# Performance work log

Measured on AMD Instinct MI355X. Metric: run time of the kernel, lower is better.

The kernel has to match this reference:

```python
import jax, jax.numpy as jnp
import numpy as np

EMBED, HEADS, LEVELS, POINTS, MLP = 256, 8, 3, 4, 4
SHAPES = [(60, 80), (30, 40), (15, 20)]  # (H, W) per level


def layer_norm(x, g, b):
    m = jnp.mean(x, -1, keepdims=True)
    v = jnp.mean((x - m) ** 2, -1, keepdims=True)
    return (x - m) * jax.lax.rsqrt(v + 1e-5) * g + b


def _bilinear(v, H, W, gx, gy):
    # v: [B,h,H*W,dh]; gx,gy: [B,h,Nq,P] absolute pixel coords (grid_sample align_corners=False, zero padding)
    x0 = jnp.floor(gx); y0 = jnp.floor(gy)
    wx = gx - x0; wy = gy - y0

    def g(xi, yi):
        valid = ((xi >= 0) & (xi < W) & (yi >= 0) & (yi < H)).astype(v.dtype)
        idx = jnp.clip(yi, 0, H - 1) * W + jnp.clip(xi, 0, W - 1)
        B, h, Nq, P = idx.shape
        out = jnp.take_along_axis(v, idx.reshape(B, h, Nq * P)[..., None], axis=2)
        return out.reshape(B, h, Nq, P, -1) * valid[..., None]

    x0i = x0.astype(jnp.int32); y0i = y0.astype(jnp.int32)
    return (g(x0i, y0i) * ((1 - wx) * (1 - wy))[..., None]
            + g(x0i + 1, y0i) * (wx * (1 - wy))[..., None]
            + g(x0i, y0i + 1) * ((1 - wx) * wy)[..., None]
            + g(x0i + 1, y0i + 1) * (wx * wy)[..., None])


def setup_inputs() -> dict:
    key = jax.random.key(0)
    ks = jax.random.split(key, 16)
    B, Nq, C = 2, 8192, EMBED
    Nv = sum(h * w for h, w in SHAPES)
    s = 0.02
    d = {
        'query': jax.random.normal(ks[0], (B, Nq, C), jnp.float32),
        'value': jax.random.normal(ks[1], (B, Nv, C), jnp.float32),
        'query_pos': jax.random.normal(ks[2], (B, Nq, C), jnp.float32),
        'ref_pts': jax.random.uniform(ks[3], (B, Nq, LEVELS, 2), jnp.float32),
        'spatial_shapes': jnp.array(SHAPES, jnp.int32),
        'level_start_index': jnp.array(np.cumsum([0] + [h * w for h, w in SHAPES[:-1]]), jnp.int32),
        'g1': jnp.ones((C,), jnp.float32), 'b1': jnp.zeros((C,), jnp.float32),
        'Wo': s * jax.random.normal(ks[4], (C, HEADS * LEVELS * POINTS * 2), jnp.float32),
        'bo': jnp.zeros((HEADS * LEVELS * POINTS * 2,), jnp.float32),
        'Wa': s * jax.random.normal(ks[5], (C, HEADS * LEVELS * POINTS), jnp.float32),
        'ba': jnp.zeros((HEADS * LEVELS * POINTS,), jnp.float32),
        'Wv': s * jax.random.normal(ks[6], (C, C), jnp.float32), 'bv': jnp.zeros((C,), jnp.float32),
        'Wp': s * jax.random.normal(ks[7], (C, C), jnp.float32), 'bp': jnp.zeros((C,), jnp.float32),
        'g2': jnp.ones((C,), jnp.float32), 'b2': jnp.zeros((C,), jnp.float32),
        'Wf1': s * jax.random.normal(ks[8], (C, MLP * C), jnp.float32), 'bf1': jnp.zeros((MLP * C,), jnp.float32),
        'Wf2': s * jax.random.normal(ks[9], (MLP * C, C), jnp.float32), 'bf2': jnp.zeros((C,), jnp.float32),
    }
    return d


def reference(query, value, query_pos, ref_pts, spatial_shapes, level_start_index,
              g1, b1, Wo, bo, Wa, ba, Wv, bv, Wp, bp, g2, b2, Wf1, bf1, Wf2, bf2):
    B, Nq, C = query.shape
    dh = C // HEADS
    shapes = np.asarray(spatial_shapes).tolist()
    starts = np.asarray(level_start_index).tolist()

    qn = layer_norm(query, g1, b1)           # pre-norm
    qa = qn + query_pos                       # positional embedding inside attn
    offs = (qa @ Wo + bo).reshape(B, Nq, HEADS, LEVELS, POINTS, 2)
    aw = jax.nn.softmax((qa @ Wa + ba).reshape(B, Nq, HEADS, LEVELS * POINTS), -1)
    aw = aw.reshape(B, Nq, HEADS, LEVELS, POINTS)
    v = (value @ Wv + bv).reshape(B, -1, HEADS, dh).transpose(0, 2, 1, 3)  # [B,h,Nv,dh]

    # offset_normalizer = (W, H) per level
    norm = jnp.array([[w, h] for h, w in shapes], jnp.float32)
    loc = ref_pts[:, :, None, :, None, :] + offs / norm[None, None, None, :, None, :]

    out = jnp.zeros((B, Nq, HEADS, dh), query.dtype)
    for l, (H, W) in enumerate(shapes):
        vl = jax.lax.dynamic_slice_in_dim(v, starts[l], H * W, axis=2)
        gl = loc[:, :, :, l].transpose(0, 2, 1, 3, 4)   # [B,h,Nq,P,2]
        gx = gl[..., 0] * W - 0.5
        gy = gl[..., 1] * H - 0.5
        sampled = _bilinear(vl, H, W, gx, gy)            # [B,h,Nq,P,dh]
        out = out + jnp.einsum('bhqpd,bqhp->bqhd', sampled, aw[:, :, :, l])

    attn = out.reshape(B, Nq, C) @ Wp + bp + qn          # output proj + mmcv internal residual (identity=norm1(query))
    q = query + attn                                     # layer residual
    q2 = layer_norm(q, g2, b2)
    return q + (jax.nn.gelu(q2 @ Wf1 + bf1, approximate=False) @ Wf2 + bf2)
```

## Files before the change

### kernel.cpp

```cpp
#include <hip/hip_runtime.h>
#include <math.h>


typedef short short8 __attribute__((ext_vector_type(8)));
typedef short s16x4 __attribute__((ext_vector_type(4)));
typedef __bf16 bf16x8 __attribute__((ext_vector_type(8)));
typedef float f32x4 __attribute__((ext_vector_type(4)));

__device__ __forceinline__ short f2b(float f) {
  unsigned u = __builtin_bit_cast(unsigned, f);
  u += 0x7fffu + ((u >> 16) & 1u);
  return (short)(u >> 16);
}
__device__ __forceinline__ float b2f(short s) {
  unsigned u = ((unsigned)(unsigned short)s) << 16;
  return __builtin_bit_cast(float, u);
}
__device__ __forceinline__ void b8f(short8 s, float* f) {
  const uint4 u = __builtin_bit_cast(uint4, s);
  f[0] = __builtin_bit_cast(float, u.x << 16);
  f[1] = __builtin_bit_cast(float, u.x & 0xffff0000u);
  f[2] = __builtin_bit_cast(float, u.y << 16);
  f[3] = __builtin_bit_cast(float, u.y & 0xffff0000u);
  f[4] = __builtin_bit_cast(float, u.z << 16);
  f[5] = __builtin_bit_cast(float, u.z & 0xffff0000u);
  f[6] = __builtin_bit_cast(float, u.w << 16);
  f[7] = __builtin_bit_cast(float, u.w & 0xffff0000u);
}

__device__ __forceinline__ f32x4 mfma16(short8 a, short8 b, f32x4 c) {
  return __builtin_amdgcn_mfma_f32_16x16x32_bf16(
      __builtin_bit_cast(bf16x8, a), __builtin_bit_cast(bf16x8, b), c, 0, 0, 0);
}

typedef __attribute__((address_space(3))) unsigned int lds_u32;
typedef const __attribute__((address_space(1))) unsigned int glb_u32;
__device__ __forceinline__ void glds16(const void* g, void* l) {
  __builtin_amdgcn_global_load_lds((glb_u32*)g, (lds_u32*)l, 16, 0, 0);
}

__device__ __forceinline__ float gelu1(float v) {
  return 0.5f * v * (1.f + erff(v * 0.70710678118654752f));
}

template <int EPI>
__device__ __forceinline__ void gemm_core(
    int bx, int by,
    const short* __restrict__ A, const short* __restrict__ Bt,
    const float* __restrict__ bias, const float* __restrict__ bias2,
    const void* __restrict__ add1, const float* __restrict__ add2,
    void* __restrict__ Cout, int M, int Nreal, int ldc, int K, char* smem)
{
  short* sA = (short*)smem;
  short* sB = sA + 8192;
  float* sf = (float*)smem;

  const int t = threadIdx.x;
  const int wave = t >> 6, lane = t & 63;
  const int quad = lane >> 4, l16 = lane & 15;
  const int wm = (wave & 1) * 64, wn = (wave >> 1) * 64;
  const int m0 = by * 128, n0 = bx * 128;

  f32x4 acc[4][4];
#pragma unroll
  for (int i = 0; i < 4; i++)
#pragma unroll
    for (int j = 0; j < 4; j++) acc[i][j] = (f32x4){0.f, 0.f, 0.f, 0.f};

  const int srow = lane >> 3, pos = lane & 7;
  const int chunk = (pos + srow) & 7;
  const short* gA = A + (size_t)(m0 + wave * 32 + srow) * K + chunk * 8;
  const short* gB = Bt + (size_t)(n0 + wave * 32 + srow) * K + chunk * 8;

  const int nk = K >> 6;
  for (int kt = 0; kt < nk; ++kt) {
    if (kt) __syncthreads();
    const int ko = kt * 64;
#pragma unroll
    for (int g = 0; g < 4; ++g) {
      glds16(gA + ko + (size_t)(g * 8) * K, sA + (wave * 32 + g * 8) * 64);
      glds16(gB + ko + (size_t)(g * 8) * K, sB + (wave * 32 + g * 8) * 64);
    }
    __syncthreads();
#pragma unroll
    for (int kk = 0; kk < 2; ++kk) {
      short8 af[4], bf[4];
      const int c = kk * 4 + quad;
#pragma unroll
      for (int i = 0; i < 4; i++) {
        const int lrA = wm + i * 16 + l16;
        af[i] = *(const short8*)&sA[lrA * 64 + ((c - lrA) & 7) * 8];
        const int lrB = wn + i * 16 + l16;
        bf[i] = *(const short8*)&sB[lrB * 64 + ((c - lrB) & 7) * 8];
      }
#pragma unroll
      for (int i = 0; i < 4; i++)
#pragma unroll
        for (int j = 0; j < 4; j++) acc[i][j] = mfma16(bf[j], af[i], acc[i][j]);
    }
  }
  __syncthreads();

#pragma unroll
  for (int b = 0; b < 4; ++b) {
    const bool mine = (b < 2) ? (wm == 0) : (wm == 64);
    if (mine) {
#pragma unroll
      for (int ii = 0; ii < 2; ++ii) {
        const int i = (b & 1) * 2 + ii;
        const int rr = ii * 16 + l16;
#pragma unroll
        for (int j = 0; j < 4; ++j)
          *(f32x4*)&sf[rr * 132 + wn + quad * 4 + j * 16] = acc[i][j];
      }
    }
    __syncthreads();
#pragma unroll
    for (int r2 = 0; r2 < 4; ++r2) {
      const int fidx = r2 * 1024 + t * 4;
      const int row = fidx >> 7, col = fidx & 127;
      const int gm = m0 + b * 32 + row;
      const int cc = n0 + col;
      if (gm < M && cc < Nreal) {
        const float4 v = *(const float4*)&sf[row * 132 + col];
        float4 bb;
        if (EPI == 4) bb = (cc < 192) ? *(const float4*)(bias + cc)
                                      : *(const float4*)(bias2 + cc - 192);
        else bb = *(const float4*)(bias + cc);
        float v0 = v.x + bb.x, v1 = v.y + bb.y, v2 = v.z + bb.z, v3 = v.w + bb.w;
        if (EPI == 1) {
          v0 = gelu1(v0); v1 = gelu1(v1); v2 = gelu1(v2); v3 = gelu1(v3);
          s16x4 o; o.x = f2b(v0); o.y = f2b(v1); o.z = f2b(v2); o.w = f2b(v3);
          *(s16x4*)((short*)Cout + (size_t)gm * ldc + cc) = o;
        } else if (EPI == 5) {
          s16x4 o; o.x = f2b(v0); o.y = f2b(v1); o.z = f2b(v2); o.w = f2b(v3);
          *(s16x4*)((short*)Cout + (size_t)gm * ldc + cc) = o;
        } else {
          if (EPI == 2) {
            const s16x4 a1 = *(const s16x4*)((const short*)add1 + (size_t)gm * ldc + cc);
            v0 += b2f(a1.x); v1 += b2f(a1.y); v2 += b2f(a1.z); v3 += b2f(a1.w);
            const float4 a2 = *(const float4*)(add2 + (size_t)gm * ldc + cc);
            v0 += a2.x; v1 += a2.y; v2 += a2.z; v3 += a2.w;
          } else if (EPI == 3) {
            const float4 a1 = *(const float4*)((const float*)add1 + (size_t)gm * ldc + cc);
            v0 += a1.x; v1 += a1.y; v2 += a1.z; v3 += a1.w;
          }
          *(float4*)((float*)Cout + (size_t)gm * ldc + cc) =
              make_float4(v0, v1, v2, v3);
        }
      }
    }
    __syncthreads();
  }
}

template <int EPI>
__global__ __launch_bounds__(256) void gemm_k(
    const short* __restrict__ A, const short* __restrict__ Bt,
    const float* __restrict__ bias, const float* __restrict__ bias2,
    const void* __restrict__ add1, const float* __restrict__ add2,
    void* __restrict__ Cout, int M, int Nreal, int ldc, int K)
{
  __shared__ __align__(16) char smem[32768];
  gemm_core<EPI>(blockIdx.x, blockIdx.y, A, Bt, bias, bias2, add1, add2,
                 Cout, M, Nreal, ldc, K, smem);
}

__global__ __launch_bounds__(256) void gemm_oa_v(
    const short* __restrict__ qa, const short* __restrict__ wt_oa,
    const float* __restrict__ bo, const float* __restrict__ ba,
    float* __restrict__ oabuf,
    const short* __restrict__ valbf, const short* __restrict__ wt_v,
    const float* __restrict__ bv, short* __restrict__ vproj)
{
  __shared__ __align__(16) char smem[32768];
  const int idx = blockIdx.x;
  if (idx < 384) {
    gemm_core<4>(idx % 3, idx / 3, qa, wt_oa, bo, ba, nullptr, nullptr,
                 oabuf, 16384, 288, 288, 256, smem);
  } else {
    const int r = idx - 384;
    gemm_core<5>(r % 2, r / 2, valbf, wt_v, bv, nullptr, nullptr, nullptr,
                 vproj, 12600, 256, 256, 256, smem);
  }
}

__global__ __launch_bounds__(256) void prep_all(
    const float* __restrict__ Wo, const float* __restrict__ Wa,
    const float* __restrict__ Wv, const float* __restrict__ Wp,
    const float* __restrict__ Wf1, const float* __restrict__ Wf2,
    short* __restrict__ t_oa, short* __restrict__ t_v, short* __restrict__ t_p,
    short* __restrict__ t_f1, short* __restrict__ t_f2,
    const float* __restrict__ value, short* __restrict__ valbf,
    const float* __restrict__ query, const float* __restrict__ query_pos,
    const float* __restrict__ g1, const float* __restrict__ b1,
    short* __restrict__ qnb, short* __restrict__ qa)
{
  __shared__ float tile[32][33];
  const int t = threadIdx.x;
  const int blk = blockIdx.x;

  if (blk < 1792) {
    const int bxa = blk & 255, bya = blk >> 8;
    int K, N, noff; const float* src; short* dst;
    switch (bya) {
      case 0: src = Wo;      dst = t_oa; K = 256;  N = 192;  noff = 0;   break;
      case 1: src = Wa;      dst = t_oa; K = 256;  N = 96;   noff = 192; break;
      case 2: src = nullptr; dst = t_oa; K = 256;  N = 96;   noff = 288; break;
      case 3: src = Wv;      dst = t_v;  K = 256;  N = 256;  noff = 0;   break;
      case 4: src = Wp;      dst = t_p;  K = 256;  N = 256;  noff = 0;   break;
      case 5: src = Wf1;     dst = t_f1; K = 256;  N = 1024; noff = 0;   break;
      default: src = Wf2;    dst = t_f2; K = 1024; N = 256;  noff = 0;   break;
    }
    const int tilesK = K >> 5;
    const int nt = tilesK * (N >> 5);
    if (bxa >= nt) return;
    const int tk = bxa % tilesK, tn = bxa / tilesK;
    const int k0 = tk * 32, n0 = tn * 32;
    const int r = t >> 3, c4 = (t & 7) * 4;
    float4 v = make_float4(0.f, 0.f, 0.f, 0.f);
    if (src) v = *(const float4*)(src + (size_t)(k0 + r) * N + n0 + c4);
    tile[r][c4] = v.x; tile[r][c4 + 1] = v.y; tile[r][c4 + 2] = v.z; tile[r][c4 + 3] = v.w;
    __syncthreads();
    const int nn = t >> 3, kc = (t & 7) * 4;
    s16x4 o;
    o.x = f2b(tile[kc][nn]); o.y = f2b(tile[kc + 1][nn]);
    o.z = f2b(tile[kc + 2][nn]); o.w = f2b(tile[kc + 3][nn]);
    *(s16x4*)(dst + (size_t)(noff + n0 + nn) * K + k0 + kc) = o;
  } else if (blk < 1792 + 3169) {
    const int i = ((blk - 1792) * 256 + t) * 4;
    if (i >= 12672 * 256) return;
    s16x4 o = (s16x4){0, 0, 0, 0};
    if (i < 12600 * 256) {
      float4 v = *(const float4*)(value + i);
      o.x = f2b(v.x); o.y = f2b(v.y); o.z = f2b(v.z); o.w = f2b(v.w);
    }
    *(s16x4*)(valbf + i) = o;
  } else {
    const int row  = (blk - 4961) * 4 + (t >> 6);
    const int lane = t & 63;
    const float4 v = ((const float4*)(query + (size_t)row * 256))[lane];
    float s = v.x + v.y + v.z + v.w;
#pragma unroll
    for (int o = 32; o; o >>= 1) s += __shfl_xor(s, o);
    const float mean = s * (1.f / 256.f);
    const float dx = v.x - mean, dy = v.y - mean, dz = v.z - mean, dw = v.w - mean;
    float s2 = dx * dx + dy * dy + dz * dz + dw * dw;
#pragma unroll
    for (int o = 32; o; o >>= 1) s2 += __shfl_xor(s2, o);
    const float inv = rsqrtf(s2 * (1.f / 256.f) + 1e-5f);
    const float4 gv = ((const float4*)g1)[lane];
    const float4 bv = ((const float4*)b1)[lane];
    const float4 o1 = make_float4(dx * inv * gv.x + bv.x, dy * inv * gv.y + bv.y,
                                  dz * inv * gv.z + bv.z, dw * inv * gv.w + bv.w);
    s16x4 ob; ob.x = f2b(o1.x); ob.y = f2b(o1.y); ob.z = f2b(o1.z); ob.w = f2b(o1.w);
    ((s16x4*)(qnb + (size_t)row * 256))[lane] = ob;
    const float4 pv = ((const float4*)(query_pos + (size_t)row * 256))[lane];
    s16x4 op;
    op.x = f2b(o1.x + pv.x); op.y = f2b(o1.y + pv.y);
    op.z = f2b(o1.z + pv.z); op.w = f2b(o1.w + pv.w);
    ((s16x4*)(qa + (size_t)row * 256))[lane] = op;
  }
}

__global__ __launch_bounds__(256) void ln_kernel(
    const float* __restrict__ x, const float* __restrict__ g,
    const float* __restrict__ bta, short* __restrict__ yb)
{
  const int row  = blockIdx.x * 4 + (threadIdx.x >> 6);
  const int lane = threadIdx.x & 63;
  const float4 v = ((const float4*)(x + (size_t)row * 256))[lane];
  float s = v.x + v.y + v.z + v.w;
#pragma unroll
  for (int o = 32; o; o >>= 1) s += __shfl_xor(s, o);
  const float mean = s * (1.f / 256.f);
  const float dx = v.x - mean, dy = v.y - mean, dz = v.z - mean, dw = v.w - mean;
  float s2 = dx * dx + dy * dy + dz * dz + dw * dw;
#pragma unroll
  for (int o = 32; o; o >>= 1) s2 += __shfl_xor(s2, o);
  const float inv = rsqrtf(s2 * (1.f / 256.f) + 1e-5f);
  const float4 gv = ((const float4*)g)[lane];
  const float4 bv = ((const float4*)bta)[lane];
  s16x4 ob;
  ob.x = f2b(dx * inv * gv.x + bv.x); ob.y = f2b(dy * inv * gv.y + bv.y);
  ob.z = f2b(dz * inv * gv.z + bv.z); ob.w = f2b(dw * inv * gv.w + bv.w);
  ((s16x4*)(yb + (size_t)row * 256))[lane] = ob;
}

__global__ __launch_bounds__(256) void deform_fused(
    const short* __restrict__ vproj, const float* __restrict__ oa,
    const float* __restrict__ refp, short* __restrict__ out)
{
  __shared__ int4 sIdx[768];
  __shared__ s16x4 sW[768];
  const int t = threadIdx.x;

  if (t < 64) {
    const int row = blockIdx.x * 8 + (t >> 3), h = t & 7;
    const float* oarow = oa + (size_t)row * 288;
    float off[24];
    const float4* op = (const float4*)(oarow + h * 24);
#pragma unroll
    for (int i = 0; i < 6; i++) {
      const float4 v = op[i];
      off[i * 4] = v.x; off[i * 4 + 1] = v.y; off[i * 4 + 2] = v.z; off[i * 4 + 3] = v.w;
    }
    float lg[12];
    const float4* ap = (const float4*)(oarow + 192 + h * 12);
#pragma unroll
    for (int i = 0; i < 3; i++) {
      const float4 v = ap[i];
      lg[i * 4] = v.x; lg[i * 4 + 1] = v.y; lg[i * 4 + 2] = v.z; lg[i * 4 + 3] = v.w;
    }
    const float* rp = refp + (size_t)row * 6;
    const float Rx[3] = {rp[0], rp[2], rp[4]}, Ry[3] = {rp[1], rp[3], rp[5]};
    float mx = lg[0];
#pragma unroll
    for (int i = 1; i < 12; i++) mx = fmaxf(mx, lg[i]);
    float sum = 0.f;
#pragma unroll
    for (int i = 0; i < 12; i++) { lg[i] = __expf(lg[i] - mx); sum += lg[i]; }
    const float inv = 1.f / sum;
    const int b = row >> 13;
    const int Hs[3] = {60, 30, 15}, Ws[3] = {80, 40, 20}, St[3] = {0, 4800, 6000};
#pragma unroll
    for (int p = 0; p < 12; p++) {
      const int l = p >> 2;
      const int W = Ws[l], H = Hs[l];
      const float gx = Rx[l] * W + off[p * 2]     - 0.5f;
      const float gy = Ry[l] * H + off[p * 2 + 1] - 0.5f;
      const float x0f = floorf(gx), y0f = floorf(gy);
      const float wx = gx - x0f, wy = gy - y0f;
      const int x0 = (int)x0f, y0 = (int)y0f;
      const float aw = lg[p] * inv;
      float cw[4] = {(1.f - wx) * (1.f - wy), wx * (1.f - wy),
                     (1.f - wx) * wy, wx * wy};
      const int base = b * 6300 + St[l];
      int ci[4];
#pragma unroll
      for (int k = 0; k < 4; k++) {
        const int xx = x0 + (k & 1), yy = y0 + (k >> 1);
        const bool valid = (xx >= 0) & (xx < W) & (yy >= 0) & (yy < H);
        const int xc = min(max(xx, 0), W - 1);
        const int yc = min(max(yy, 0), H - 1);
        ci[k] = ((base + yc * W + xc) << 8) + h * 32;
        cw[k] = valid ? cw[k] * aw : 0.f;
      }
      sIdx[t * 12 + p] = make_int4(ci[0], ci[1], ci[2], ci[3]);
      s16x4 wv; wv.x = f2b(cw[0]); wv.y = f2b(cw[1]); wv.z = f2b(cw[2]); wv.w = f2b(cw[3]);
      sW[t * 12 + p] = wv;
    }
  }
  __syncthreads();

  const int lu = t >> 2, c4 = (t & 3) * 8;
  float acc[8];
#pragma unroll
  for (int i = 0; i < 8; i++) acc[i] = 0.f;
#pragma unroll 2
  for (int p = 0; p < 12; p++) {
    const int4 idx = sIdx[lu * 12 + p];
    const s16x4 wb = sW[lu * 12 + p];
    const float w0 = b2f(wb.x), w1 = b2f(wb.y), w2 = b2f(wb.z), w3 = b2f(wb.w);
    const short8 v0 = *(const short8*)(vproj + idx.x + c4);
    const short8 v1 = *(const short8*)(vproj + idx.y + c4);
    const short8 v2 = *(const short8*)(vproj + idx.z + c4);
    const short8 v3 = *(const short8*)(vproj + idx.w + c4);
    float f0[8], f1[8], f2[8], f3[8];
    b8f(v0, f0); b8f(v1, f1); b8f(v2, f2); b8f(v3, f3);
#pragma unroll
    for (int j = 0; j < 8; j++)
      acc[j] += w0 * f0[j] + w1 * f1[j] + w2 * f2[j] + w3 * f3[j];
  }
  short8 o;
#pragma unroll
  for (int j = 0; j < 8; j++) o[j] = f2b(acc[j]);
  *(short8*)(out + (size_t)(blockIdx.x * 256 + t) * 8) = o;
}

extern "C" void kernel_launch(void* const* d_in, const int* in_sizes, int n_in,
                              void* d_out, int out_size, void* d_ws, size_t ws_size,
                              hipStream_t stream)
{
  const float* query     = (const float*)d_in[0];
  const float* value     = (const float*)d_in[1];
  const float* query_pos = (const float*)d_in[2];
  const float* ref_pts   = (const float*)d_in[3];
  const float* g1  = (const float*)d_in[6];
  const float* b1  = (const float*)d_in[7];
  const float* Wo  = (const float*)d_in[8];
  const float* bo  = (const float*)d_in[9];
  const float* Wa  = (const float*)d_in[10];
  const float* ba  = (const float*)d_in[11];
  const float* Wv  = (const float*)d_in[12];
  const float* bv  = (const float*)d_in[13];
  const float* Wp  = (const float*)d_in[14];
  const float* bp  = (const float*)d_in[15];
  const float* g2  = (const float*)d_in[16];
  const float* b2  = (const float*)d_in[17];
  const float* Wf1 = (const float*)d_in[18];
  const float* bf1 = (const float*)d_in[19];
  const float* Wf2 = (const float*)d_in[20];
  const float* bf2 = (const float*)d_in[21];

  char* ws = (char*)d_ws;
  short* wt_oa   = (short*)(ws + 0);
  short* wt_v    = (short*)(ws + 196608);
  short* wt_p    = (short*)(ws + 327680);
  short* wt_f1   = (short*)(ws + 458752);
  short* wt_f2   = (short*)(ws + 983040);
  short* qnb     = (short*)(ws + 1507328);
  short* qa      = (short*)(ws + 18284544);
  float* oabuf   = (float*)(ws + 26673152);
  short* vproj   = (short*)(ws + 45547520);
  short* sampled = (short*)(ws + 51998720);
  float* qbuf    = (float*)(ws + 60387328);
  short* valbf   = (short*)(ws + 77164544);
  short* q2      = qa;
  short* hidden  = (short*)(ws + 26673152);
  float* outp = (float*)d_out;

  prep_all<<<9057, 256, 0, stream>>>(Wo, Wa, Wv, Wp, Wf1, Wf2,
                                     wt_oa, wt_v, wt_p, wt_f1, wt_f2,
                                     value, valbf, query, query_pos,
                                     g1, b1, qnb, qa);
  gemm_oa_v<<<582, 256, 0, stream>>>(qa, wt_oa, bo, ba, oabuf,
                                     valbf, wt_v, bv, vproj);
  deform_fused<<<2048, 256, 0, stream>>>(vproj, oabuf, ref_pts, sampled);
  gemm_k<2><<<dim3(2, 128), 256, 0, stream>>>(sampled, wt_p, bp, nullptr, qnb,
                                              query, qbuf, 16384, 256, 256, 256);
  ln_kernel<<<4096, 256, 0, stream>>>(qbuf, g2, b2, q2);
  gemm_k<1><<<dim3(8, 128), 256, 0, stream>>>(q2, wt_f1, bf1, nullptr, nullptr,
                                              nullptr, hidden, 16384, 1024, 1024, 256);
  gemm_k<3><<<dim3(2, 128), 256, 0, stream>>>(hidden, wt_f2, bf2, nullptr, qbuf,
                                              nullptr, outp, 16384, 256, 256, 1024);
}
```

Baseline: 239.0 us.

## Fuse output projection with LayerNorm and widen FFN1 GEMM tile

Adds a dedicated output-projection GEMM in which each block owns 64 full rows of 256 columns, so the bias, residual adds and the second LayerNorm are computed in the epilogue. This removes the separate LN kernel and one fp32 round trip through qbuf. It also adds a specialised FFN1 GEMM with 128x256 tiles and a GELU epilogue, which halves its grid and raises reuse per block. The cost is larger LDS use per block (about 65KB and 48KB) and a grid of only 256 blocks for the fused projection, both of which can lower occupancy.

After: 261.9 us. 1.1x slower.

```diff
diff --git a/kernel.cpp b/kernel.cpp
--- a/kernel.cpp
+++ b/kernel.cpp
@@ -48,7 +48,7 @@
     int bx, int by,
     const short* __restrict__ A, const short* __restrict__ Bt,
     const float* __restrict__ bias, const float* __restrict__ bias2,
-    const void* __restrict__ add1, const float* __restrict__ add2,
+    const void* __restrict__ add1,
     void* __restrict__ Cout, int M, int Nreal, int ldc, int K, char* smem)
 {
   short* sA = (short*)smem;
@@ -136,12 +136,7 @@
           s16x4 o; o.x = f2b(v0); o.y = f2b(v1); o.z = f2b(v2); o.w = f2b(v3);
           *(s16x4*)((short*)Cout + (size_t)gm * ldc + cc) = o;
         } else {
-          if (EPI == 2) {
-            const s16x4 a1 = *(const s16x4*)((const short*)add1 + (size_t)gm * ldc + cc);
-            v0 += b2f(a1.x); v1 += b2f(a1.y); v2 += b2f(a1.z); v3 += b2f(a1.w);
-            const float4 a2 = *(const float4*)(add2 + (size_t)gm * ldc + cc);
-            v0 += a2.x; v1 += a2.y; v2 += a2.z; v3 += a2.w;
-          } else if (EPI == 3) {
+          if (EPI == 3) {
             const float4 a1 = *(const float4*)((const float*)add1 + (size_t)gm * ldc + cc);
             v0 += a1.x; v1 += a1.y; v2 += a1.z; v3 += a1.w;
           }
@@ -157,12 +152,11 @@
 template <int EPI>
 __global__ __launch_bounds__(256) void gemm_k(
     const short* __restrict__ A, const short* __restrict__ Bt,
-    const float* __restrict__ bias, const float* __restrict__ bias2,
-    const void* __restrict__ add1, const float* __restrict__ add2,
+    const float* __restrict__ bias, const void* __restrict__ add1,
     void* __restrict__ Cout, int M, int Nreal, int ldc, int K)
 {
   __shared__ __align__(16) char smem[32768];
-  gemm_core<EPI>(blockIdx.x, blockIdx.y, A, Bt, bias, bias2, add1, add2,
+  gemm_core<EPI>(blockIdx.x, blockIdx.y, A, Bt, bias, nullptr, add1,
                  Cout, M, Nreal, ldc, K, smem);
 }
 
@@ -176,12 +170,200 @@
   __shared__ __align__(16) char smem[32768];
   const int idx = blockIdx.x;
   if (idx < 384) {
-    gemm_core<4>(idx % 3, idx / 3, qa, wt_oa, bo, ba, nullptr, nullptr,
+    gemm_core<4>(idx % 3, idx / 3, qa, wt_oa, bo, ba, nullptr,
                  oabuf, 16384, 288, 288, 256, smem);
   } else {
     const int r = idx - 384;
-    gemm_core<5>(r % 2, r / 2, valbf, wt_v, bv, nullptr, nullptr, nullptr,
+    gemm_core<5>(r % 2, r / 2, valbf, wt_v, bv, nullptr, nullptr,
                  vproj, 12600, 256, 256, 256, smem);
+  }
+}
+
+__global__ __launch_bounds__(256) void gemm_wp_ln(
+    const short* __restrict__ A, const short* __restrict__ Bt,
+    const float* __restrict__ bias,
+    const short* __restrict__ qnb, const float* __restrict__ query,
+    const float* __restrict__ g2, const float* __restrict__ b2v,
+    float* __restrict__ qbuf, short* __restrict__ q2)
+{
+  __shared__ __align__(16) char smem[66560];
+  short* sA = (short*)smem;
+  short* sB = sA + 4096;
+  float* sf = (float*)smem;
+
+  const int t = threadIdx.x;
+  const int wave = t >> 6, lane = t & 63;
+  const int quad = lane >> 4, l16 = lane & 15;
+  const int wn = wave * 64;
+  const int m0 = blockIdx.x * 64;
+  const int K = 256;
+
+  f32x4 acc[4][4];
+#pragma unroll
+  for (int i = 0; i < 4; i++)
+#pragma unroll
+    for (int j = 0; j < 4; j++) acc[i][j] = (f32x4){0.f, 0.f, 0.f, 0.f};
+
+  const int srow = lane >> 3, pos = lane & 7;
+  const int chunk = (pos + srow) & 7;
+  const short* gA = A + (size_t)(m0 + wave * 16 + srow) * K + chunk * 8;
+  const short* gB = Bt + (size_t)(wave * 64 + srow) * K + chunk * 8;
+
+  for (int kt = 0; kt < 4; ++kt) {
+    if (kt) __syncthreads();
+    const int ko = kt * 64;
+#pragma unroll
+    for (int g = 0; g < 2; ++g)
+      glds16(gA + ko + (size_t)(g * 8) * K, sA + (wave * 16 + g * 8) * 64);
+#pragma unroll
+    for (int g = 0; g < 8; ++g)
+      glds16(gB + ko + (size_t)(g * 8) * K, sB + (wave * 64 + g * 8) * 64);
+    __syncthreads();
+#pragma unroll
+    for (int kk = 0; kk < 2; ++kk) {
+      short8 af[4], bf[4];
+      const int c = kk * 4 + quad;
+#pragma unroll
+      for (int i = 0; i < 4; i++) {
+        const int lrA = i * 16 + l16;
+        af[i] = *(const short8*)&sA[lrA * 64 + ((c - lrA) & 7) * 8];
+        const int lrB = wn + i * 16 + l16;
+        bf[i] = *(const short8*)&sB[lrB * 64 + ((c - lrB) & 7) * 8];
+      }
+#pragma unroll
+      for (int i = 0; i < 4; i++)
+#pragma unroll
+        for (int j = 0; j < 4; j++) acc[i][j] = mfma16(bf[j], af[i], acc[i][j]);
+    }
+  }
+  __syncthreads();
+
+#pragma unroll
+  for (int i = 0; i < 4; i++)
+#pragma unroll
+    for (int j = 0; j < 4; j++)
+      *(f32x4*)&sf[(i * 16 + l16) * 260 + wn + j * 16 + quad * 4] = acc[i][j];
+  __syncthreads();
+
+  const float4 bb = *(const float4*)(bias + lane * 4);
+  const float4 gv = *(const float4*)(g2 + lane * 4);
+  const float4 b2f4 = *(const float4*)(b2v + lane * 4);
+#pragma unroll 4
+  for (int rr = 0; rr < 16; ++rr) {
+    const int row = wave * 16 + rr;
+    const int gm = m0 + row;
+    const float4 a = *(const float4*)&sf[row * 260 + lane * 4];
+    const s16x4 qn = *(const s16x4*)(qnb + (size_t)gm * 256 + lane * 4);
+    const float4 qv = *(const float4*)(query + (size_t)gm * 256 + lane * 4);
+    float q0 = a.x + bb.x + b2f(qn.x) + qv.x;
+    float q1 = a.y + bb.y + b2f(qn.y) + qv.y;
+    float q2f = a.z + bb.z + b2f(qn.z) + qv.z;
+    float q3 = a.w + bb.w + b2f(qn.w) + qv.w;
+    float s = q0 + q1 + q2f + q3;
+#pragma unroll
+    for (int o = 32; o; o >>= 1) s += __shfl_xor(s, o);
+    const float mean = s * (1.f / 256.f);
+    const float d0 = q0 - mean, d1 = q1 - mean, d2 = q2f - mean, d3 = q3 - mean;
+    float ss = d0 * d0 + d1 * d1 + d2 * d2 + d3 * d3;
+#pragma unroll
+    for (int o = 32; o; o >>= 1) ss += __shfl_xor(ss, o);
+    const float inv = rsqrtf(ss * (1.f / 256.f) + 1e-5f);
+    *(float4*)(qbuf + (size_t)gm * 256 + lane * 4) = make_float4(q0, q1, q2f, q3);
+    s16x4 o2;
+    o2.x = f2b(d0 * inv * gv.x + b2f4.x);
+    o2.y = f2b(d1 * inv * gv.y + b2f4.y);
+    o2.z = f2b(d2 * inv * gv.z + b2f4.z);
+    o2.w = f2b(d3 * inv * gv.w + b2f4.w);
+    *(s16x4*)(q2 + (size_t)gm * 256 + lane * 4) = o2;
+  }
+}
+
+__global__ __launch_bounds__(256) void gemm_f1(
+    const short* __restrict__ A, const short* __restrict__ Bt,
+    const float* __restrict__ bias, short* __restrict__ Cout)
+{
+  __shared__ __align__(16) char smem[49152];
+  short* sA = (short*)smem;
+  short* sB = sA + 8192;
+  float* sf = (float*)smem;
+
+  const int t = threadIdx.x;
+  const int wave = t >> 6, lane = t & 63;
+  const int quad = lane >> 4, l16 = lane & 15;
+  const int wm = (wave & 1) * 64, wn = (wave >> 1) * 128;
+  const int m0 = blockIdx.y * 128, n0 = blockIdx.x * 256;
+  const int K = 256;
+
+  f32x4 acc[4][8];
+#pragma unroll
+  for (int i = 0; i < 4; i++)
+#pragma unroll
+    for (int j = 0; j < 8; j++) acc[i][j] = (f32x4){0.f, 0.f, 0.f, 0.f};
+
+  const int srow = lane >> 3, pos = lane & 7;
+  const int chunk = (pos + srow) & 7;
+  const short* gA = A + (size_t)(m0 + wave * 32 + srow) * K + chunk * 8;
+  const short* gB = Bt + (size_t)(n0 + wave * 64 + srow) * K + chunk * 8;
+
+  for (int kt = 0; kt < 4; ++kt) {
+    if (kt) __syncthreads();
+    const int ko = kt * 64;
+#pragma unroll
+    for (int g = 0; g < 4; ++g)
+      glds16(gA + ko + (size_t)(g * 8) * K, sA + (wave * 32 + g * 8) * 64);
+#pragma unroll
+    for (int g = 0; g < 8; ++g)
+      glds16(gB + ko + (size_t)(g * 8) * K, sB + (wave * 64 + g * 8) * 64);
+    __syncthreads();
+#pragma unroll
+    for (int kk = 0; kk < 2; ++kk) {
+      short8 af[4], bf[8];
+      const int c = kk * 4 + quad;
+#pragma unroll
+      for (int i = 0; i < 4; i++) {
+        const int lrA = wm + i * 16 + l16;
+        af[i] = *(const short8*)&sA[lrA * 64 + ((c - lrA) & 7) * 8];
+      }
+#pragma unroll
+      for (int j = 0; j < 8; j++) {
+        const int lrB = wn + j * 16 + l16;
+        bf[j] = *(const short8*)&sB[lrB * 64 + ((c - lrB) & 7) * 8];
+      }
+#pragma unroll
+      for (int i = 0; i < 4; i++)
+#pragma unroll
+        for (int j = 0; j < 8; j++) acc[i][j] = mfma16(bf[j], af[i], acc[i][j]);
+    }
+  }
+  __syncthreads();
+
+#pragma unroll
+  for (int b = 0; b < 4; ++b) {
+    if ((wave & 1) == (b >> 1)) {
+#pragma unroll
+      for (int ii = 0; ii < 2; ++ii) {
+        const int i = (b & 1) * 2 + ii;
+        const int rr = ii * 16 + l16;
+#pragma unroll
+        for (int j = 0; j < 8; ++j)
+          *(f32x4*)&sf[rr * 260 + wn + j * 16 + quad * 4] = acc[i][j];
+      }
+    }
+    __syncthreads();
+#pragma unroll
+    for (int it = 0; it < 8; ++it) {
+      const int fidx = it * 1024 + t * 4;
+      const int row = fidx >> 8, col = fidx & 255;
+      const int gm = m0 + b * 32 + row;
+      const int cc = n0 + col;
+      const float4 v = *(const float4*)&sf[row * 260 + col];
+      const float4 bb = *(const float4*)(bias + cc);
+      float v0 = gelu1(v.x + bb.x), v1 = gelu1(v.y + bb.y);
+      float v2 = gelu1(v.z + bb.z), v3 = gelu1(v.w + bb.w);
+      s16x4 o; o.x = f2b(v0); o.y = f2b(v1); o.z = f2b(v2); o.w = f2b(v3);
+      *(s16x4*)(Cout + (size_t)gm * 1024 + cc) = o;
+    }
+    __syncthreads();
   }
 }
 
@@ -261,30 +443,6 @@
     op.z = f2b(o1.z + pv.z); op.w = f2b(o1.w + pv.w);
     ((s16x4*)(qa + (size_t)row * 256))[lane] = op;
   }
-}
-
-__global__ __launch_bounds__(256) void ln_kernel(
-    const float* __restrict__ x, const float* __restrict__ g,
-    const float* __restrict__ bta, short* __restrict__ yb)
-{
-  const int row  = blockIdx.x * 4 + (threadIdx.x >> 6);
-  const int lane = threadIdx.x & 63;
-  const float4 v = ((const float4*)(x + (size_t)row * 256))[lane];
-  float s = v.x + v.y + v.z + v.w;
-#pragma unroll
-  for (int o = 32; o; o >>= 1) s += __shfl_xor(s, o);
-  const float mean = s * (1.f / 256.f);
-  const float dx = v.x - mean, dy = v.y - mean, dz = v.z - mean, dw = v.w - mean;
-  float s2 = dx * dx + dy * dy + dz * dz + dw * dw;
-#pragma unroll
-  for (int o = 32; o; o >>= 1) s2 += __shfl_xor(s2, o);
-  const float inv = rsqrtf(s2 * (1.f / 256.f) + 1e-5f);
-  const float4 gv = ((const float4*)g)[lane];
-  const float4 bv = ((const float4*)bta)[lane];
-  s16x4 ob;
-  ob.x = f2b(dx * inv * gv.x + bv.x); ob.y = f2b(dy * inv * gv.y + bv.y);
-  ob.z = f2b(dz * inv * gv.z + bv.z); ob.w = f2b(dw * inv * gv.w + bv.w);
-  ((s16x4*)(yb + (size_t)row * 256))[lane] = ob;
 }
 
 __global__ __launch_bounds__(256) void deform_fused(
@@ -427,11 +585,9 @@
   gemm_oa_v<<<582, 256, 0, stream>>>(qa, wt_oa, bo, ba, oabuf,
                                      valbf, wt_v, bv, vproj);
   deform_fused<<<2048, 256, 0, stream>>>(vproj, oabuf, ref_pts, sampled);
-  gemm_k<2><<<dim3(2, 128), 256, 0, stream>>>(sampled, wt_p, bp, nullptr, qnb,
-                                              query, qbuf, 16384, 256, 256, 256);
-  ln_kernel<<<4096, 256, 0, stream>>>(qbuf, g2, b2, q2);
-  gemm_k<1><<<dim3(8, 128), 256, 0, stream>>>(q2, wt_f1, bf1, nullptr, nullptr,
-                                              nullptr, hidden, 16384, 1024, 1024, 256);
-  gemm_k<3><<<dim3(2, 128), 256, 0, stream>>>(hidden, wt_f2, bf2, nullptr, qbuf,
-                                              nullptr, outp, 16384, 256, 256, 1024);
-}
+  gemm_wp_ln<<<256, 256, 0, stream>>>(sampled, wt_p, bp, qnb, query,
+                                      g2, b2, qbuf, q2);
+  gemm_f1<<<dim3(4, 128), 256, 0, stream>>>(q2, wt_f1, bf1, hidden);
+  gemm_k<3><<<dim3(2, 128), 256, 0, stream>>>(hidden, wt_f2, bf2, qbuf,
+                                              outp, 16384, 256, 256, 1024);
+}
```
